# Performance work log

Hardware: AMD Instinct MI355X
Metric: run time of the kernel (lower is better)

The kernel has to match this reference:

```python
import jax, jax.numpy as jnp
import numpy as np

H = 1024
I = 4096
E = 8
B, S, K = 2, 2048, 2


def setup_inputs() -> dict:
    key = jax.random.key(0)
    k1, k2, k3, k4, k5, k6 = jax.random.split(key, 6)
    x = jax.random.normal(k1, (B, S, H), dtype=jnp.float32)
    expert_indices = jax.random.randint(k2, (B, S, K), 0, E, dtype=jnp.int32)
    expert_weights = jax.random.uniform(k3, (B, S, K), dtype=jnp.float32)
    gate_proj = jax.random.normal(k4, (E, I, H), dtype=jnp.float32) * 0.02
    up_proj = jax.random.normal(k5, (E, I, H), dtype=jnp.float32) * 0.02
    down_proj = jax.random.normal(k6, (E, H, I), dtype=jnp.float32) * 0.02
    return {"x": x, "expert_indices": expert_indices, "expert_weights": expert_weights,
            "gate_proj": gate_proj, "up_proj": up_proj, "down_proj": down_proj}


def reference(x, expert_indices, expert_weights, gate_proj, up_proj, down_proj):
    b, s, h = x.shape
    e = gate_proj.shape[0]
    k = expert_indices.shape[-1]
    xf = x.reshape(-1, h)                       # [N, H]
    idx = expert_indices.reshape(-1, k)         # [N, K]
    wts = expert_weights.reshape(-1, k)         # [N, K]
    # combine[n, e] = sum over slots k with idx[n,k]==e of wts[n,k]
    onehot = jax.nn.one_hot(idx, e, dtype=x.dtype)            # [N, K, E]
    combine = jnp.einsum('nk,nke->ne', wts, onehot)           # [N, E]
    out = jnp.zeros_like(xf)
    # Fixed small unrolled loop over experts (data dims fully vectorized).
    for ei in range(e):
        gate = jax.nn.silu(xf @ gate_proj[ei].T)              # [N, I]
        up = xf @ up_proj[ei].T                               # [N, I]
        out = out + ((gate * up) @ down_proj[ei].T) * combine[:, ei:ei + 1]
    return out.reshape(b, s, h)
```

## Files before the change

kernel.cpp:

```cpp
#include <hip/hip_runtime.h>
#include <hip/hip_bf16.h>
#include <cstdint>

#define HD 1024
#define ID 4096
#define NE 8
#define NTOK 4096
#define NASS 8192
#define NWL 72

typedef unsigned short u16;
typedef __attribute__((ext_vector_type(8))) __bf16 bf16x8;
typedef __attribute__((ext_vector_type(4))) float f32x4;

__device__ __forceinline__ void async16(void* lds, const void* g) {
  __builtin_amdgcn_global_load_lds(
      (const __attribute__((address_space(1))) uint32_t*)g,
      (__attribute__((address_space(3))) uint32_t*)lds, 16, 0, 0);
}

__device__ __forceinline__ u16 f2b(float f) {
  __bf16 h = (__bf16)f;
  return __builtin_bit_cast(u16, h);
}

__device__ __forceinline__ bf16x8 cvt8(const float* p) {
  const float4* q = (const float4*)p;
  float4 a = q[0], b = q[1];
  bf16x8 v;
  v[0] = (__bf16)a.x; v[1] = (__bf16)a.y; v[2] = (__bf16)a.z; v[3] = (__bf16)a.w;
  v[4] = (__bf16)b.x; v[5] = (__bf16)b.y; v[6] = (__bf16)b.z; v[7] = (__bf16)b.w;
  return v;
}

__global__ void k_pre(const float* __restrict__ x, const float* __restrict__ gate,
                      const float* __restrict__ up, const float* __restrict__ down,
                      u16* __restrict__ xb, u16* __restrict__ wg,
                      u16* __restrict__ wu, u16* __restrict__ wd) {
  int bid = blockIdx.x, t = threadIdx.x;
  const float* src; u16* dst; size_t base;
  if (bid < 2048)        { src = x;    dst = xb; base = (size_t)bid * 256; }
  else if (bid < 18432)  { src = gate; dst = wg; base = (size_t)(bid - 2048) * 256; }
  else if (bid < 34816)  { src = up;   dst = wu; base = (size_t)(bid - 18432) * 256; }
  else                   { src = down; dst = wd; base = (size_t)(bid - 34816) * 256; }
  size_t i8 = (base + t) * 8;
  *(bf16x8*)(dst + i8) = cvt8(src + i8);
}

__global__ void k_meta(const int* __restrict__ eidx, int* __restrict__ offsets,
                       int* __restrict__ wl, int* __restrict__ tokl) {
  __shared__ int cnt[NE], offs_s[NE + 1], cur[NE];
  int t = threadIdx.x;
  if (t < NE) cnt[t] = 0;
  __syncthreads();
  for (int i = t; i < NASS; i += 1024) atomicAdd(&cnt[eidx[i]], 1);
  __syncthreads();
  if (t == 0) {
    int s = 0;
    for (int e = 0; e < NE; ++e) { offs_s[e] = s; s += cnt[e]; }
    offs_s[NE] = s;
    int w = 0;
    for (int e = 0; e < NE; ++e)
      for (int mt = 0; mt * 128 < cnt[e]; ++mt) wl[w++] = (e << 16) | mt;
    for (; w < NWL; ++w) wl[w] = -1;
  }
  if (t < NE) cur[t] = 0;
  __syncthreads();
  for (int i = t; i < NASS; i += 1024) {
    int e = eidx[i];
    int p = atomicAdd(&cur[e], 1);
    tokl[offs_s[e] + p] = i;
  }
  if (t <= NE) offsets[t] = offs_s[t];
}

__global__ __launch_bounds__(256) void k_g1(
    const u16* __restrict__ xb, const u16* __restrict__ wg, const u16* __restrict__ wu,
    const int* __restrict__ offsets, const int* __restrict__ wl,
    const int* __restrict__ tokl, u16* __restrict__ interm) {
  const int wle = wl[blockIdx.y];
  if (wle < 0) return;
  const int e = wle >> 16;
  const int m0 = (wle & 0xffff) << 7;
  const int offs = offsets[e];
  const int Me = offsets[e + 1] - offs;
  const int n0 = blockIdx.x * 64;
  const int t = threadIdx.x, lane = t & 63, wv = t >> 6;
  const int wm = wv & 1, wn = wv >> 1;

  __shared__ __align__(16) u16 As[128 * 64];
  __shared__ __align__(16) u16 Bg[64 * 64];
  __shared__ __align__(16) u16 Bu[64 * 64];

  const u16* asrc[4];
#pragma unroll
  for (int p = 0; p < 4; ++p) {
    int c = p * 256 + t;
    int r = c >> 3, c8 = c & 7;
    int row = m0 + r; if (row > Me - 1) row = Me - 1;
    asrc[p] = xb + (size_t)(tokl[offs + row] >> 1) * HD + c8 * 8;
  }
  const u16 *bgsrc[2], *busrc[2];
#pragma unroll
  for (int q = 0; q < 2; ++q) {
    int c = q * 256 + t;
    int r = c >> 3, c8 = c & 7;
    size_t boff = ((size_t)e * ID + n0 + r) * HD + c8 * 8;
    bgsrc[q] = wg + boff;
    busrc[q] = wu + boff;
  }

  f32x4 accg[4][2], accu[4][2];
#pragma unroll
  for (int mi = 0; mi < 4; ++mi)
#pragma unroll
    for (int ni = 0; ni < 2; ++ni) {
      accg[mi][ni] = (f32x4){0.f, 0.f, 0.f, 0.f};
      accu[mi][ni] = (f32x4){0.f, 0.f, 0.f, 0.f};
    }

  const int lrow = lane & 15, lk = (lane >> 4) * 8;
#pragma unroll 1
  for (int ks = 0; ks < HD / 64; ++ks) {
    __syncthreads();
#pragma unroll
    for (int p = 0; p < 4; ++p)
      async16((char*)As + (p * 256 + wv * 64) * 16, asrc[p]);
#pragma unroll
    for (int q = 0; q < 2; ++q) {
      async16((char*)Bg + (q * 256 + wv * 64) * 16, bgsrc[q]);
      async16((char*)Bu + (q * 256 + wv * 64) * 16, busrc[q]);
    }
    __syncthreads();
#pragma unroll
    for (int kk = 0; kk < 2; ++kk) {
      bf16x8 af[4], bg[2], bu[2];
#pragma unroll
      for (int mi = 0; mi < 4; ++mi)
        af[mi] = *(const bf16x8*)&As[(wm * 64 + mi * 16 + lrow) * 64 + kk * 32 + lk];
#pragma unroll
      for (int ni = 0; ni < 2; ++ni) {
        bg[ni] = *(const bf16x8*)&Bg[(wn * 32 + ni * 16 + lrow) * 64 + kk * 32 + lk];
        bu[ni] = *(const bf16x8*)&Bu[(wn * 32 + ni * 16 + lrow) * 64 + kk * 32 + lk];
      }
#pragma unroll
      for (int mi = 0; mi < 4; ++mi)
#pragma unroll
        for (int ni = 0; ni < 2; ++ni) {
          accg[mi][ni] = __builtin_amdgcn_mfma_f32_16x16x32_bf16(af[mi], bg[ni], accg[mi][ni], 0, 0, 0);
          accu[mi][ni] = __builtin_amdgcn_mfma_f32_16x16x32_bf16(af[mi], bu[ni], accu[mi][ni], 0, 0, 0);
        }
    }
#pragma unroll
    for (int p = 0; p < 4; ++p) asrc[p] += 64;
    bgsrc[0] += 64; bgsrc[1] += 64; busrc[0] += 64; busrc[1] += 64;
  }

#pragma unroll
  for (int mi = 0; mi < 4; ++mi) {
    int rb = wm * 64 + mi * 16 + (lane >> 4) * 4;
#pragma unroll
    for (int ni = 0; ni < 2; ++ni) {
      int col = n0 + wn * 32 + ni * 16 + (lane & 15);
#pragma unroll
      for (int j = 0; j < 4; ++j) {
        int row = m0 + rb + j;
        if (row < Me) {
          float g = accg[mi][ni][j], u = accu[mi][ni][j];
          float s = g / (1.f + __expf(-g));
          interm[(size_t)(offs + row) * ID + col] = f2b(s * u);
        }
      }
    }
  }
}

__global__ __launch_bounds__(256) void k_g2(
    const u16* __restrict__ interm, const u16* __restrict__ wd,
    const int* __restrict__ offsets, const int* __restrict__ wl,
    const int* __restrict__ tokl, float* __restrict__ buf) {
  const int wle = wl[blockIdx.y];
  if (wle < 0) return;
  const int e = wle >> 16;
  const int m0 = (wle & 0xffff) << 7;
  const int offs = offsets[e];
  const int Me = offsets[e + 1] - offs;
  const int n0 = blockIdx.x * 128;
  const int t = threadIdx.x, lane = t & 63, wv = t >> 6;
  const int wm = wv & 1, wn = wv >> 1;

  __shared__ __align__(16) u16 As[128 * 64];
  __shared__ __align__(16) u16 Bs[128 * 64];

  const u16* asrc[4];
#pragma unroll
  for (int p = 0; p < 4; ++p) {
    int c = p * 256 + t;
    int r = c >> 3, c8 = c & 7;
    int row = m0 + r; if (row > Me - 1) row = Me - 1;
    asrc[p] = interm + (size_t)(offs + row) * ID + c8 * 8;
  }
  const u16* bsrc[4];
#pragma unroll
  for (int p = 0; p < 4; ++p) {
    int c = p * 256 + t;
    int r = c >> 3, c8 = c & 7;
    bsrc[p] = wd + ((size_t)e * HD + n0 + r) * ID + c8 * 8;
  }

  f32x4 acc[4][4];
#pragma unroll
  for (int mi = 0; mi < 4; ++mi)
#pragma unroll
    for (int ni = 0; ni < 4; ++ni) acc[mi][ni] = (f32x4){0.f, 0.f, 0.f, 0.f};

  const int lrow = lane & 15, lk = (lane >> 4) * 8;
#pragma unroll 1
  for (int ks = 0; ks < ID / 64; ++ks) {
    __syncthreads();
#pragma unroll
    for (int p = 0; p < 4; ++p) {
      async16((char*)As + (p * 256 + wv * 64) * 16, asrc[p]);
      async16((char*)Bs + (p * 256 + wv * 64) * 16, bsrc[p]);
    }
    __syncthreads();
#pragma unroll
    for (int kk = 0; kk < 2; ++kk) {
      bf16x8 af[4], bfr[4];
#pragma unroll
      for (int mi = 0; mi < 4; ++mi)
        af[mi] = *(const bf16x8*)&As[(wm * 64 + mi * 16 + lrow) * 64 + kk * 32 + lk];
#pragma unroll
      for (int ni = 0; ni < 4; ++ni)
        bfr[ni] = *(const bf16x8*)&Bs[(wn * 64 + ni * 16 + lrow) * 64 + kk * 32 + lk];
#pragma unroll
      for (int mi = 0; mi < 4; ++mi)
#pragma unroll
        for (int ni = 0; ni < 4; ++ni)
          acc[mi][ni] = __builtin_amdgcn_mfma_f32_16x16x32_bf16(af[mi], bfr[ni], acc[mi][ni], 0, 0, 0);
    }
#pragma unroll
    for (int p = 0; p < 4; ++p) { asrc[p] += 64; bsrc[p] += 64; }
  }

#pragma unroll
  for (int mi = 0; mi < 4; ++mi) {
    int rb = wm * 64 + mi * 16 + (lane >> 4) * 4;
#pragma unroll
    for (int j = 0; j < 4; ++j) {
      int row = m0 + rb + j;
      if (row < Me) {
        int aid = tokl[offs + row];
#pragma unroll
        for (int ni = 0; ni < 4; ++ni) {
          int col = n0 + wn * 64 + ni * 16 + (lane & 15);
          buf[(size_t)aid * HD + col] = acc[mi][ni][j];
        }
      }
    }
  }
}

__global__ void k_final(const float* __restrict__ buf, const float* __restrict__ ewt,
                        float* __restrict__ out) {
  size_t idx = (size_t)blockIdx.x * 256 + threadIdx.x;
  int tok = (int)(idx >> 8);
  int c4 = (int)(idx & 255);
  const float4* b0 = (const float4*)(buf + (size_t)(2 * tok) * HD) + c4;
  const float4* b1 = (const float4*)(buf + (size_t)(2 * tok + 1) * HD) + c4;
  float w0 = ewt[2 * tok], w1 = ewt[2 * tok + 1];
  float4 a = *b0, b = *b1;
  float4 r = {w0 * a.x + w1 * b.x, w0 * a.y + w1 * b.y,
              w0 * a.z + w1 * b.z, w0 * a.w + w1 * b.w};
  ((float4*)(out + (size_t)tok * HD))[c4] = r;
}

extern "C" void kernel_launch(void* const* d_in, const int* in_sizes, int n_in,
                              void* d_out, int out_size, void* d_ws, size_t ws_size,
                              hipStream_t stream) {
  const float* x    = (const float*)d_in[0];
  const int*   eidx = (const int*)d_in[1];
  const float* ewt  = (const float*)d_in[2];
  const float* gate = (const float*)d_in[3];
  const float* up   = (const float*)d_in[4];
  const float* down = (const float*)d_in[5];
  float* out = (float*)d_out;
  char* ws = (char*)d_ws;

  constexpr size_t OFF_INTERM = 0;
  constexpr size_t OFF_XB     = 67108864;
  constexpr size_t OFF_META   = 75497472;
  constexpr size_t OFF_TOK    = 75498496;
  constexpr size_t OFF_WD     = 75531264;
  constexpr size_t OFF_WG     = 142640128;
  constexpr size_t OFF_WU     = 209748992;

  u16* interm  = (u16*)(ws + OFF_INTERM);
  u16* xb      = (u16*)(ws + OFF_XB);
  int* offsets = (int*)(ws + OFF_META);
  int* wl      = (int*)(ws + OFF_META + 64);
  int* tokl    = (int*)(ws + OFF_TOK);
  u16* wd      = (u16*)(ws + OFF_WD);
  u16* wg      = (u16*)(ws + OFF_WG);
  u16* wu      = (u16*)(ws + OFF_WU);
  float* buf   = (float*)(ws + OFF_WG);

  k_pre<<<dim3(51200), dim3(256), 0, stream>>>(x, gate, up, down, xb, wg, wu, wd);
  k_meta<<<dim3(1), dim3(1024), 0, stream>>>(eidx, offsets, wl, tokl);
  k_g1<<<dim3(ID / 64, NWL), dim3(256), 0, stream>>>(xb, wg, wu, offsets, wl, tokl, interm);
  k_g2<<<dim3(HD / 128, NWL), dim3(256), 0, stream>>>(interm, wd, offsets, wl, tokl, buf);
  k_final<<<dim3(4096), dim3(256), 0, stream>>>(buf, ewt, out);
}
```

Baseline: 553.5 us.

## Widen g1 N-tile to 128 and overlap down_proj conversion inside g1 grid

After: 483.9 us. -12.6%, faster.

```diff
diff --git a/kernel.cpp b/kernel.cpp
--- a/kernel.cpp
+++ b/kernel.cpp
@@ -34,15 +34,13 @@
 }
 
 __global__ void k_pre(const float* __restrict__ x, const float* __restrict__ gate,
-                      const float* __restrict__ up, const float* __restrict__ down,
-                      u16* __restrict__ xb, u16* __restrict__ wg,
-                      u16* __restrict__ wu, u16* __restrict__ wd) {
+                      const float* __restrict__ up, u16* __restrict__ xb,
+                      u16* __restrict__ wg, u16* __restrict__ wu) {
   int bid = blockIdx.x, t = threadIdx.x;
   const float* src; u16* dst; size_t base;
   if (bid < 2048)        { src = x;    dst = xb; base = (size_t)bid * 256; }
   else if (bid < 18432)  { src = gate; dst = wg; base = (size_t)(bid - 2048) * 256; }
-  else if (bid < 34816)  { src = up;   dst = wu; base = (size_t)(bid - 18432) * 256; }
-  else                   { src = down; dst = wd; base = (size_t)(bid - 34816) * 256; }
+  else                   { src = up;   dst = wu; base = (size_t)(bid - 18432) * 256; }
   size_t i8 = (base + t) * 8;
   *(bf16x8*)(dst + i8) = cvt8(src + i8);
 }
@@ -74,23 +72,37 @@
   if (t <= NE) offsets[t] = offs_s[t];
 }
 
-__global__ __launch_bounds__(256) void k_g1(
+__global__ __launch_bounds__(256, 2) void k_g1(
     const u16* __restrict__ xb, const u16* __restrict__ wg, const u16* __restrict__ wu,
+    const float* __restrict__ down, u16* __restrict__ wd,
     const int* __restrict__ offsets, const int* __restrict__ wl,
     const int* __restrict__ tokl, u16* __restrict__ interm) {
+  const int bx = blockIdx.x;
+  const int t = threadIdx.x;
+  if (bx >= 32) {
+    int cid = (bx - 32) + 32 * (int)blockIdx.y;
+    if (cid < 2048) {
+#pragma unroll
+      for (int l = 0; l < 8; ++l) {
+        size_t i8 = (((size_t)cid * 8 + l) * 256 + t) * 8;
+        *(bf16x8*)(wd + i8) = cvt8(down + i8);
+      }
+    }
+    return;
+  }
   const int wle = wl[blockIdx.y];
   if (wle < 0) return;
   const int e = wle >> 16;
   const int m0 = (wle & 0xffff) << 7;
   const int offs = offsets[e];
   const int Me = offsets[e + 1] - offs;
-  const int n0 = blockIdx.x * 64;
-  const int t = threadIdx.x, lane = t & 63, wv = t >> 6;
+  const int n0 = bx * 128;
+  const int lane = t & 63, wv = t >> 6;
   const int wm = wv & 1, wn = wv >> 1;
 
   __shared__ __align__(16) u16 As[128 * 64];
-  __shared__ __align__(16) u16 Bg[64 * 64];
-  __shared__ __align__(16) u16 Bu[64 * 64];
+  __shared__ __align__(16) u16 Bg[128 * 64];
+  __shared__ __align__(16) u16 Bu[128 * 64];
 
   const u16* asrc[4];
 #pragma unroll
@@ -100,21 +112,21 @@
     int row = m0 + r; if (row > Me - 1) row = Me - 1;
     asrc[p] = xb + (size_t)(tokl[offs + row] >> 1) * HD + c8 * 8;
   }
-  const u16 *bgsrc[2], *busrc[2];
-#pragma unroll
-  for (int q = 0; q < 2; ++q) {
-    int c = q * 256 + t;
+  const u16 *bgsrc[4], *busrc[4];
+#pragma unroll
+  for (int p = 0; p < 4; ++p) {
+    int c = p * 256 + t;
     int r = c >> 3, c8 = c & 7;
     size_t boff = ((size_t)e * ID + n0 + r) * HD + c8 * 8;
-    bgsrc[q] = wg + boff;
-    busrc[q] = wu + boff;
-  }
-
-  f32x4 accg[4][2], accu[4][2];
+    bgsrc[p] = wg + boff;
+    busrc[p] = wu + boff;
+  }
+
+  f32x4 accg[4][4], accu[4][4];
 #pragma unroll
   for (int mi = 0; mi < 4; ++mi)
 #pragma unroll
-    for (int ni = 0; ni < 2; ++ni) {
+    for (int ni = 0; ni < 4; ++ni) {
       accg[mi][ni] = (f32x4){0.f, 0.f, 0.f, 0.f};
       accu[mi][ni] = (f32x4){0.f, 0.f, 0.f, 0.f};
     }
@@ -124,44 +136,41 @@
   for (int ks = 0; ks < HD / 64; ++ks) {
     __syncthreads();
 #pragma unroll
-    for (int p = 0; p < 4; ++p)
+    for (int p = 0; p < 4; ++p) {
       async16((char*)As + (p * 256 + wv * 64) * 16, asrc[p]);
-#pragma unroll
-    for (int q = 0; q < 2; ++q) {
-      async16((char*)Bg + (q * 256 + wv * 64) * 16, bgsrc[q]);
-      async16((char*)Bu + (q * 256 + wv * 64) * 16, busrc[q]);
+      async16((char*)Bg + (p * 256 + wv * 64) * 16, bgsrc[p]);
+      async16((char*)Bu + (p * 256 + wv * 64) * 16, busrc[p]);
     }
     __syncthreads();
 #pragma unroll
     for (int kk = 0; kk < 2; ++kk) {
-      bf16x8 af[4], bg[2], bu[2];
+      bf16x8 af[4], bg[4], bu[4];
 #pragma unroll
       for (int mi = 0; mi < 4; ++mi)
         af[mi] = *(const bf16x8*)&As[(wm * 64 + mi * 16 + lrow) * 64 + kk * 32 + lk];
 #pragma unroll
-      for (int ni = 0; ni < 2; ++ni) {
-        bg[ni] = *(const bf16x8*)&Bg[(wn * 32 + ni * 16 + lrow) * 64 + kk * 32 + lk];
-        bu[ni] = *(const bf16x8*)&Bu[(wn * 32 + ni * 16 + lrow) * 64 + kk * 32 + lk];
+      for (int ni = 0; ni < 4; ++ni) {
+        bg[ni] = *(const bf16x8*)&Bg[(wn * 64 + ni * 16 + lrow) * 64 + kk * 32 + lk];
+        bu[ni] = *(const bf16x8*)&Bu[(wn * 64 + ni * 16 + lrow) * 64 + kk * 32 + lk];
       }
 #pragma unroll
       for (int mi = 0; mi < 4; ++mi)
 #pragma unroll
-        for (int ni = 0; ni < 2; ++ni) {
+        for (int ni = 0; ni < 4; ++ni) {
           accg[mi][ni] = __builtin_amdgcn_mfma_f32_16x16x32_bf16(af[mi], bg[ni], accg[mi][ni], 0, 0, 0);
           accu[mi][ni] = __builtin_amdgcn_mfma_f32_16x16x32_bf16(af[mi], bu[ni], accu[mi][ni], 0, 0, 0);
         }
     }
 #pragma unroll
-    for (int p = 0; p < 4; ++p) asrc[p] += 64;
-    bgsrc[0] += 64; bgsrc[1] += 64; busrc[0] += 64; busrc[1] += 64;
+    for (int p = 0; p < 4; ++p) { asrc[p] += 64; bgsrc[p] += 64; busrc[p] += 64; }
   }
 
 #pragma unroll
   for (int mi = 0; mi < 4; ++mi) {
     int rb = wm * 64 + mi * 16 + (lane >> 4) * 4;
 #pragma unroll
-    for (int ni = 0; ni < 2; ++ni) {
-      int col = n0 + wn * 32 + ni * 16 + (lane & 15);
+    for (int ni = 0; ni < 4; ++ni) {
+      int col = n0 + wn * 64 + ni * 16 + (lane & 15);
 #pragma unroll
       for (int j = 0; j < 4; ++j) {
         int row = m0 + rb + j;
@@ -305,9 +314,9 @@
   u16* wu      = (u16*)(ws + OFF_WU);
   float* buf   = (float*)(ws + OFF_WG);
 
-  k_pre<<<dim3(51200), dim3(256), 0, stream>>>(x, gate, up, down, xb, wg, wu, wd);
+  k_pre<<<dim3(34816), dim3(256), 0, stream>>>(x, gate, up, xb, wg, wu);
   k_meta<<<dim3(1), dim3(1024), 0, stream>>>(eidx, offsets, wl, tokl);
-  k_g1<<<dim3(ID / 64, NWL), dim3(256), 0, stream>>>(xb, wg, wu, offsets, wl, tokl, interm);
+  k_g1<<<dim3(64, NWL), dim3(256), 0, stream>>>(xb, wg, wu, down, wd, offsets, wl, tokl, interm);
   k_g2<<<dim3(HD / 128, NWL), dim3(256), 0, stream>>>(interm, wd, offsets, wl, tokl, buf);
   k_final<<<dim3(4096), dim3(256), 0, stream>>>(buf, ewt, out);
 }
```
